# Kernel optimization log

Measured on AMD Instinct MI355X. Metric: run time of the kernel, lower is better.

Reference implementation:

```python
import jax, jax.numpy as jnp
import numpy as np

N_G, E_G = 76800, 307200   # gg: line graph over bonds
N_L, E_L = 38400, 153600   # lg: atom graph; E_L == 2*N_G
B = 64                     # number of molecules (equal-sized subgraphs)
H = 8                      # attention heads
BOND, ATOM, IN_E, FE1 = 40, 92, 10, 36


def _egat_layer(nfeats, efeats, src, dst, N, W_node, b_node, W_ni, W_nj, W_fij, attn, bias, Fn, Fe):
    # edge scores: gather + add (u_add_v) + edge proj + bias, leaky_relu
    f_edge = (nfeats @ W_ni)[src] + (nfeats @ W_nj)[dst] + efeats @ W_fij + bias
    f_out = jax.nn.leaky_relu(f_edge).reshape(-1, H, Fe)         # [E,H,Fe]
    e = jnp.einsum('ehf,hf->eh', f_out, attn)                     # [E,H]
    # edge softmax over incoming edges of each destination node
    m = jax.lax.stop_gradient(jax.ops.segment_max(e, dst, num_segments=N))
    ex = jnp.exp(e - m[dst])
    a = ex / jax.ops.segment_sum(ex, dst, num_segments=N)[dst]    # [E,H]
    h = (nfeats @ W_node + b_node).reshape(-1, H, Fn)             # [N,H,Fn]
    h_out = jax.ops.segment_sum(h[src] * a[:, :, None], dst, num_segments=N)
    return h_out, f_out


def setup_inputs() -> dict:
    key = jax.random.key(0)
    ks = iter(jax.random.split(key, 64))
    def lin(i, o):
        return jax.random.normal(next(ks), (i, o), jnp.float32) * (1.0 / np.sqrt(i))
    inp = {}
    inp['gg_src'] = jax.random.randint(next(ks), (E_G,), 0, N_G, jnp.int32)
    inp['gg_dst'] = jnp.concatenate([jnp.arange(N_G, dtype=jnp.int32),
                                     jax.random.randint(next(ks), (E_G - N_G,), 0, N_G, jnp.int32)])
    inp['gg_nfeat'] = jax.random.normal(next(ks), (N_G, BOND), jnp.float32)
    inp['gg_efeat'] = jax.random.normal(next(ks), (E_G, IN_E), jnp.float32)
    inp['lg_src'] = jax.random.randint(next(ks), (E_L,), 0, N_L, jnp.int32)
    inp['lg_dst'] = jnp.concatenate([jnp.arange(N_L, dtype=jnp.int32),
                                     jax.random.randint(next(ks), (E_L - N_L,), 0, N_L, jnp.int32)])
    inp['lg_nfeat'] = jax.random.normal(next(ks), (N_L, ATOM), jnp.float32)
    inp['lg_efeat'] = jax.random.normal(next(ks), (E_L, BOND), jnp.float32)
    # layer1 (on gg): in_node=BOND, in_edge=IN_E, out_node=BOND, out_edge=FE1
    inp['W_node1'] = lin(BOND, H * BOND); inp['b_node1'] = jnp.zeros((H * BOND,), jnp.float32)
    inp['W_ni1'] = lin(BOND, H * FE1); inp['W_nj1'] = lin(BOND, H * FE1)
    inp['W_fij1'] = lin(IN_E, H * FE1)
    inp['attn1'] = jax.random.normal(next(ks), (H, FE1), jnp.float32) * 0.1
    inp['bias1'] = jnp.zeros((H * FE1,), jnp.float32)
    # layers 2a/2b (on lg): in_node=ATOM, in_edge=BOND, out_node=ATOM, out_edge=BOND
    for sfx in ('2a', '2b'):
        inp['W_node' + sfx] = lin(ATOM, H * ATOM); inp['b_node' + sfx] = jnp.zeros((H * ATOM,), jnp.float32)
        inp['W_ni' + sfx] = lin(ATOM, H * BOND); inp['W_nj' + sfx] = lin(ATOM, H * BOND)
        inp['W_fij' + sfx] = lin(BOND, H * BOND)
        inp['attn' + sfx] = jax.random.normal(next(ks), (H, BOND), jnp.float32) * 0.1
        inp['bias' + sfx] = jnp.zeros((H * BOND,), jnp.float32)
    # Readout: Linear(128,128) + Sigmoid + Linear(128,1) + Sigmoid
    inp['Wr1'] = lin(ATOM + FE1, 128); inp['br1'] = jnp.zeros((128,), jnp.float32)
    inp['Wr2'] = lin(128, 1); inp['br2'] = jnp.zeros((1,), jnp.float32)
    return inp


def reference(gg_src, gg_dst, gg_nfeat, gg_efeat, lg_src, lg_dst, lg_nfeat, lg_efeat,
              W_node1, b_node1, W_ni1, W_nj1, W_fij1, attn1, bias1,
              W_node2a, b_node2a, W_ni2a, W_nj2a, W_fij2a, attn2a, bias2a,
              W_node2b, b_node2b, W_ni2b, W_nj2b, W_fij2b, attn2b, bias2b,
              Wr1, br1, Wr2, br2):
    # stage 1: EGAT on gg, then sum over heads
    n1, e1 = _egat_layer(gg_nfeat, gg_efeat, gg_src, gg_dst, N_G,
                         W_node1, b_node1, W_ni1, W_nj1, W_fij1, attn1, bias1, BOND, FE1)
    y2n = n1.sum(axis=1)       # [N_G, BOND]
    y22 = e1.sum(axis=1)       # [E_G, FE1]
    # each gg-node feature repeated twice, added to lg edge features
    ef = jnp.repeat(y2n, 2, axis=0) + lg_efeat   # [E_L, BOND]
    nf = lg_nfeat
    nf, e2 = _egat_layer(nf, ef, lg_src, lg_dst, N_L,
                         W_node2a, b_node2a, W_ni2a, W_nj2a, W_fij2a, attn2a, bias2a, ATOM, BOND)
    nf = nf.sum(axis=1); ef = e2.sum(axis=1)
    nf, e2 = _egat_layer(nf, ef, lg_src, lg_dst, N_L,
                         W_node2b, b_node2b, W_ni2b, W_nj2b, W_fij2b, attn2b, bias2b, ATOM, BOND)
    nf = nf.sum(axis=1)
    # per-subgraph average pooling (equal-size subgraphs -> reshape mean).
    # NOTE: original pool_subgraphs(y_22, gg) slices an edge-indexed tensor by node
    # counts (upstream quirk); reproduced exactly by taking the first N_G rows.
    y1 = nf.reshape(B, N_L // B, ATOM).mean(axis=1)          # [B, ATOM]
    y2 = y22[:N_G].reshape(B, N_G // B, FE1).mean(axis=1)    # [B, FE1]
    y = jnp.concatenate([y1, y2], axis=1)                     # [B, 128]
    h = jax.nn.sigmoid(y @ Wr1 + br1)
    return jax.nn.sigmoid(h @ Wr2 + br2)                      # [B, 1]
```

## Files before the change

### kernel.cpp

```cpp
#include <hip/hip_runtime.h>
#include <math.h>

#define NG 76800
#define EG 307200
#define NL 38400
#define EL 153600
#define NB 64
#define NH 8

typedef __attribute__((ext_vector_type(8))) short bf16x8;
typedef __attribute__((ext_vector_type(4))) float f32x4;
typedef unsigned short u16;

__device__ __forceinline__ float sigmoidf(float x) { return 1.f / (1.f + expf(-x)); }
__device__ __forceinline__ u16 f2bf(float x) {
    unsigned u = __float_as_uint(x);
    return (u16)((u + 0x7FFFu + ((u >> 16) & 1u)) >> 16);
}
__device__ __forceinline__ float bf2f(u16 v) { return __uint_as_float(((unsigned)v) << 16); }

__global__ __launch_bounds__(256) void convert_pad_kernel(const float* __restrict__ src,
                                                          u16* __restrict__ dst,
                                                          int M, int K, int Kpad) {
    int i = blockIdx.x * 256 + threadIdx.x;
    if (i >= M * Kpad) return;
    int m = i / Kpad, k = i - m * Kpad;
    dst[i] = (k < K) ? f2bf(src[(size_t)m * K + k]) : (u16)0;
}

__global__ __launch_bounds__(256) void wtrans_kernel(const float* __restrict__ W, int ldw,
                                                     u16* __restrict__ dst,
                                                     int K, int N, int Nalloc, int Kpad) {
    int i = blockIdx.x * 256 + threadIdx.x;
    if (i >= Nalloc * Kpad) return;
    int n = i / Kpad, k = i - n * Kpad;
    dst[i] = (n < N && k < K) ? f2bf(W[(size_t)k * ldw + n]) : (u16)0;
}

__global__ __launch_bounds__(256) void wtrans_hp_kernel(const float* __restrict__ W, int ldw,
                                                        u16* __restrict__ dst,
                                                        int K, int Kpad) {
    int i = blockIdx.x * 256 + threadIdx.x;
    if (i >= 320 * Kpad) return;
    int n = i / Kpad, k = i - n * Kpad;
    int hh = n / 40, f = n - hh * 40;
    float v = (k < K && f < 36) ? W[(size_t)k * ldw + hh * 36 + f] : 0.f;
    dst[i] = f2bf(v);
}

__global__ __launch_bounds__(256) void wtrans_cat_kernel(const float* __restrict__ W, int ldw,
                                                         u16* __restrict__ dst,
                                                         int Fin, int Fout, int Nalloc, int KIN) {
    int i = blockIdx.x * 256 + threadIdx.x;
    if (i >= Nalloc * KIN) return;
    int n = i / KIN, k = i - n * KIN;
    int h = k / Fin, f = k - h * Fin;
    float v = (n < Fout) ? W[(size_t)f * ldw + h * Fout + n] : 0.f;
    dst[i] = f2bf(v);
}

__global__ __launch_bounds__(256) void bias_headsum_kernel(const float* __restrict__ b,
                                                           float* __restrict__ outp,
                                                           int Fout, int H, int Npad) {
    int i = blockIdx.x * 256 + threadIdx.x;
    if (i >= Npad) return;
    float s = 0.f;
    if (i < Fout)
        for (int h = 0; h < H; ++h) s += b[h * Fout + i];
    outp[i] = s;
}

__global__ __launch_bounds__(256) void meta_kernel(const float* __restrict__ attn1,
                                                   const float* __restrict__ bias1,
                                                   const float* __restrict__ b2a,
                                                   const float* __restrict__ b2b,
                                                   float* __restrict__ attn_p1,
                                                   float* __restrict__ bias_cat1,
                                                   float* __restrict__ bias_cat2a,
                                                   float* __restrict__ bias_cat2b) {
    int i = blockIdx.x * 256 + threadIdx.x;
    if (i < 320) {
        int hh = i / 40, f = i - hh * 40;
        attn_p1[i] = (f < 36) ? attn1[hh * 36 + f] : 0.f;
    } else if (i < 960) {
        int j = i - 320;
        float v = 0.f;
        if (j < 320) {
            int hh = j / 40, f = j - hh * 40;
            v = (f < 36) ? bias1[hh * 36 + f] : 0.f;
        }
        bias_cat1[j] = v;
    } else if (i < 1600) {
        int j = i - 960;
        bias_cat2a[j] = (j < 320) ? b2a[j] : 0.f;
    } else if (i < 2240) {
        int j = i - 1600;
        bias_cat2b[j] = (j < 320) ? b2b[j] : 0.f;
    }
}

template <int KPAD>
__global__ __launch_bounds__(256) void gemm_bf_kernel(const u16* __restrict__ A,
                                                      const u16* __restrict__ Wt,
                                                      const float* __restrict__ bias,
                                                      u16* __restrict__ C, int Ncols,
                                                      int Nstride) {
    __shared__ u16 st[4][16 * 72];
    const int m0 = blockIdx.x * 64;
    const int n0 = blockIdx.y * 64;
    const int wv = threadIdx.x >> 6;
    const int lane = threadIdx.x & 63;
    const int q = lane >> 4;
    const int mr = lane & 15;

    const u16* Arow = A + (size_t)(m0 + wv * 16 + mr) * KPAD;
    f32x4 acc[4];
#pragma unroll
    for (int t = 0; t < 4; ++t) acc[t] = (f32x4){0.f, 0.f, 0.f, 0.f};

#pragma unroll
    for (int k0 = 0; k0 < KPAD; k0 += 32) {
        bf16x8 af = *(const bf16x8*)(Arow + k0 + q * 8);
#pragma unroll
        for (int t = 0; t < 4; ++t) {
            bf16x8 bv = *(const bf16x8*)(Wt + (size_t)(n0 + t * 16 + mr) * KPAD + k0 + q * 8);
            acc[t] = __builtin_amdgcn_mfma_f32_16x16x32_bf16(af, bv, acc[t], 0, 0, 0);
        }
    }

    u16* myst = st[wv];
#pragma unroll
    for (int t = 0; t < 4; ++t) {
        const int colme = n0 + t * 16 + mr;
        const float bb = (bias && colme < Ncols) ? bias[colme] : 0.f;
#pragma unroll
        for (int r = 0; r < 4; ++r)
            myst[(q * 4 + r) * 72 + t * 16 + mr] = f2bf(acc[t][r] + bb);
    }
    const int rrow = lane >> 3;
    const int rcol = (lane & 7) * 8;
    bf16x8 v0 = *(const bf16x8*)(myst + rrow * 72 + rcol);
    bf16x8 v1 = *(const bf16x8*)(myst + (rrow + 8) * 72 + rcol);
    const int gcol = n0 + rcol;
    if (gcol < Ncols) {
        const int grow = m0 + wv * 16 + rrow;
        *(bf16x8*)(C + (size_t)grow * Nstride + gcol) = v0;
        *(bf16x8*)(C + (size_t)(grow + 8) * Nstride + gcol) = v1;
    }
}

__global__ __launch_bounds__(256) void ef2a_kernel(const float* __restrict__ lg_ef,
                                                   const u16* __restrict__ y2n,
                                                   u16* __restrict__ dst) {
    int i = blockIdx.x * 256 + threadIdx.x;
    if (i >= EL * 64) return;
    int e = i >> 6, c = i & 63;
    dst[i] = (c < 40) ? f2bf(lg_ef[(size_t)e * 40 + c] + bf2f(y2n[(size_t)(e >> 1) * 40 + c]))
                      : (u16)0;
}

template <int KPAD, int FSMODE>
__global__ __launch_bounds__(128) void pe_edge_kernel(
    const u16* __restrict__ A,
    const u16* __restrict__ Wt,
    const int* __restrict__ src, const int* __restrict__ dst,
    const u16* __restrict__ Pn,
    const float* __restrict__ attn,
    float* __restrict__ esc,
    void* __restrict__ fsum,
    int e0, int CH, int fsumE) {
    __shared__ u16 pe[16][328];
    const int wv = threadIdx.x >> 6;
    const int lane = threadIdx.x & 63;
    const int q = lane >> 4;
    const int mr = lane & 15;
    const int m0 = blockIdx.x * 16;

    {
        const int t0 = wv * 10;
        const u16* Arow = A + (size_t)(m0 + mr) * KPAD;
        f32x4 acc[10];
#pragma unroll
        for (int t = 0; t < 10; ++t) acc[t] = (f32x4){0.f, 0.f, 0.f, 0.f};
#pragma unroll
        for (int k0 = 0; k0 < KPAD; k0 += 32) {
            bf16x8 af = *(const bf16x8*)(Arow + k0 + q * 8);
#pragma unroll
            for (int t = 0; t < 10; ++t) {
                bf16x8 bv = *(const bf16x8*)(Wt + (size_t)((t0 + t) * 16 + mr) * KPAD + k0 + q * 8);
                acc[t] = __builtin_amdgcn_mfma_f32_16x16x32_bf16(af, bv, acc[t], 0, 0, 0);
            }
        }
#pragma unroll
        for (int t = 0; t < 10; ++t)
#pragma unroll
            for (int r = 0; r < 4; ++r)
                pe[q * 4 + r][(t0 + t) * 16 + mr] = f2bf(acc[t][r]);
    }
    __syncthreads();

    const int lc = (lane < 40) ? lane : 39;
    const int h = lc / 5, o = lc - h * 5;
    const int c = h * 40 + o * 8;
    const bool act = (lane < 40);

    float attn_r[8];
#pragma unroll
    for (int j = 0; j < 8; ++j) attn_r[j] = attn[c + j];

    const int row0 = wv * 8;
    int e = e0 + m0 + row0;
    int s = src[e], d = dst[e];
    bf16x8 api = *(const bf16x8*)(Pn + (size_t)s * 640 + c);
    bf16x8 apj = *(const bf16x8*)(Pn + (size_t)d * 640 + 320 + c);

#pragma unroll
    for (int ei = 0; ei < 8; ++ei) {
        bf16x8 napi, napj;
        if (ei < 7) {
            const int ne = e + 1;
            const int ns = src[ne], nd = dst[ne];
            napi = *(const bf16x8*)(Pn + (size_t)ns * 640 + c);
            napj = *(const bf16x8*)(Pn + (size_t)nd * 640 + 320 + c);
        }
        const int row = row0 + ei;
        bf16x8 ape = *(const bf16x8*)(&pe[row][c]);

        float v[8];
        float ehp = 0.f;
#pragma unroll
        for (int j = 0; j < 8; ++j) {
            float x = bf2f((u16)api[j]) + bf2f((u16)apj[j]) + bf2f((u16)ape[j]);
            x = x > 0.f ? x : 0.01f * x;
            v[j] = x;
            ehp += x * attn_r[j];
        }
        float eh = 0.f;
#pragma unroll
        for (int k = 0; k < 5; ++k) eh += __shfl(ehp, h * 5 + k, 64);
        if (act && o == 0) esc[(size_t)e * 8 + h] = eh;

        if (FSMODE != 0 && e < fsumE) {
#pragma unroll
            for (int m = 4; m >= 1; m >>= 1) {
                const int p = (h ^ m) * 5 + o;
#pragma unroll
                for (int j = 0; j < 8; ++j) v[j] += __shfl(v[j], p, 64);
            }
            if (act && h == 0) {
#pragma unroll
                for (int j = 0; j < 8; ++j) {
                    const int f = o * 8 + j;
                    if (FSMODE == 1) {
                        if (f < 36) ((float*)fsum)[(size_t)e * 36 + f] = v[j];
                    } else {
                        ((u16*)fsum)[(size_t)e * 64 + f] = f2bf(v[j]);
                    }
                }
            }
        }
        if (ei < 7) {
            api = napi;
            apj = napj;
        }
        ++e;
    }
}

__global__ __launch_bounds__(256) void hist_kernel(const int* __restrict__ dst,
                                                   int* __restrict__ cnt, int E) {
    int i = blockIdx.x * 256 + threadIdx.x;
    if (i < E) atomicAdd(&cnt[dst[i]], 1);
}

__global__ __launch_bounds__(1024) void scan_block_kernel(const int* __restrict__ cnt,
                                                          int* __restrict__ excl,
                                                          int* __restrict__ bsum, int N) {
    __shared__ int sd[1024];
    const int tid = threadIdx.x;
    const int i = blockIdx.x * 1024 + tid;
    int v = (i < N) ? cnt[i] : 0;
    sd[tid] = v;
    __syncthreads();
    for (int off = 1; off < 1024; off <<= 1) {
        int t = (tid >= off) ? sd[tid - off] : 0;
        __syncthreads();
        sd[tid] += t;
        __syncthreads();
    }
    if (i < N) excl[i] = sd[tid] - v;
    if (tid == 1023) bsum[blockIdx.x] = sd[1023];
}

__global__ void scan_top_kernel(int* __restrict__ bsum, int nblk) {
    if (threadIdx.x == 0 && blockIdx.x == 0) {
        int run = 0;
        for (int b = 0; b < nblk; ++b) {
            int t = bsum[b];
            bsum[b] = run;
            run += t;
        }
    }
}

__global__ __launch_bounds__(256) void scan_add_kernel(int* __restrict__ row_ptr,
                                                       const int* __restrict__ bsum,
                                                       int N, int E) {
    int i = blockIdx.x * 256 + threadIdx.x;
    if (i < N) row_ptr[i] += bsum[i >> 10];
    if (i == 0) row_ptr[N] = E;
}

__global__ __launch_bounds__(256) void scatter_kernel(const int* __restrict__ dst,
                                                      const int* __restrict__ src,
                                                      const int* __restrict__ row_ptr,
                                                      int* __restrict__ cur,
                                                      int* __restrict__ eidx,
                                                      int* __restrict__ srcs, int E) {
    int i = blockIdx.x * 256 + threadIdx.x;
    if (i < E) {
        int d = dst[i];
        int pos = row_ptr[d] + atomicAdd(&cur[d], 1);
        eidx[pos] = i;
        srcs[pos] = src[i];
    }
}

template <int GH>
__global__ __launch_bounds__(256) void csr_softmax_kernel(
    const int* __restrict__ row_ptr, const int* __restrict__ eidx,
    const float* __restrict__ esc, float* __restrict__ wcsr, int N) {
    constexpr int NS = 64 / GH;
    const int wid = threadIdx.x >> 6;
    const int lane = threadIdx.x & 63;
    const int nid = blockIdx.x * 4 + wid;
    if (nid >= N) return;
    const int r0 = row_ptr[nid], r1 = row_ptr[nid + 1];
    const int h = lane & (GH - 1);
    const int slot = lane / GH;

    float mx = -1e30f;
    for (int i = r0 + slot; i < r1; i += NS)
        mx = fmaxf(mx, esc[(size_t)eidx[i] * GH + h]);
#pragma unroll
    for (int m = GH; m < 64; m <<= 1) mx = fmaxf(mx, __shfl_xor(mx, m, 64));

    float den = 0.f;
    for (int i = r0 + slot; i < r1; i += NS)
        den += expf(esc[(size_t)eidx[i] * GH + h] - mx);
#pragma unroll
    for (int m = GH; m < 64; m <<= 1) den += __shfl_xor(den, m, 64);
    const float rden = 1.f / den;

    for (int i = r0 + slot; i < r1; i += NS)
        wcsr[(size_t)i * GH + h] = expf(esc[(size_t)eidx[i] * GH + h] - mx) * rden;
}

template <int Fn, int GH, int NFS>
__global__ __launch_bounds__(256) void node_agg_raw_kernel(
    const int* __restrict__ row_ptr,
    const int* __restrict__ srcs,
    const float* __restrict__ wcsr,
    const u16* __restrict__ nf,
    u16* __restrict__ agg, int N) {
    constexpr int PAIRS = Fn / 2;
    const int wid = threadIdx.x >> 6;
    const int lane = threadIdx.x & 63;
    const int nid = blockIdx.x * 4 + wid;
    if (nid >= N) return;
    const int r0 = row_ptr[nid], r1 = row_ptr[nid + 1];
    const int col = 2 * lane;
    const bool act = (lane < PAIRS);

    float a0[GH], a1[GH];
#pragma unroll
    for (int h = 0; h < GH; ++h) { a0[h] = 0.f; a1[h] = 0.f; }

    for (int i = r0; i < r1; i += 4) {
        const u16* prs[4];
        float wv[4][GH];
#pragma unroll
        for (int b = 0; b < 4; ++b) {
            const int ii = (i + b < r1) ? (i + b) : (r1 - 1);
            prs[b] = nf + (size_t)srcs[ii] * NFS;
            const float live = (i + b < r1) ? 1.f : 0.f;
            const float* wp = wcsr + (size_t)ii * GH;
#pragma unroll
            for (int h = 0; h < GH; ++h) wv[b][h] = wp[h] * live;
        }
        if (act) {
            unsigned pv[4];
#pragma unroll
            for (int b = 0; b < 4; ++b) pv[b] = *(const unsigned*)(prs[b] + col);
#pragma unroll
            for (int b = 0; b < 4; ++b) {
                const float lo = bf2f((u16)(pv[b] & 0xFFFFu));
                const float hi = bf2f((u16)(pv[b] >> 16));
#pragma unroll
                for (int h = 0; h < GH; ++h) {
                    a0[h] += wv[b][h] * lo;
                    a1[h] += wv[b][h] * hi;
                }
            }
        }
    }
    if (act) {
        u16* ob = agg + (size_t)nid * (GH * Fn);
#pragma unroll
        for (int h = 0; h < GH; ++h) {
            unsigned pk = (unsigned)f2bf(a0[h]) | ((unsigned)f2bf(a1[h]) << 16);
            *(unsigned*)(ob + h * Fn + col) = pk;
        }
    }
}

__global__ __launch_bounds__(256) void readout_kernel(const u16* __restrict__ nfb,
                                                      const float* __restrict__ y22p,
                                                      const float* __restrict__ Wr1,
                                                      const float* __restrict__ br1,
                                                      const float* __restrict__ Wr2,
                                                      const float* __restrict__ br2,
                                                      float* __restrict__ out) {
    const int b = blockIdx.x;
    const int t = threadIdx.x;
    __shared__ float sA[20][96];
    __shared__ float sB[28][36];
    __shared__ float y[128];
    __shared__ float hh[128];
    __shared__ float red[128];
    if (t < 240) {
        const int cc = t % 12, rg = t / 12;
        float s[8];
#pragma unroll
        for (int j = 0; j < 8; ++j) s[j] = 0.f;
        const u16* base = nfb + (size_t)b * 600 * 96 + cc * 8;
        for (int i = rg; i < 600; i += 20) {
            bf16x8 v = *(const bf16x8*)(base + (size_t)i * 96);
#pragma unroll
            for (int j = 0; j < 8; ++j) s[j] += bf2f((u16)v[j]);
        }
#pragma unroll
        for (int j = 0; j < 8; ++j) sA[rg][cc * 8 + j] = s[j];
    }
    if (t < 252) {
        const int cc = t % 9, rg = t / 9;
        float s0 = 0.f, s1 = 0.f, s2 = 0.f, s3 = 0.f;
        const float* base = y22p + (size_t)b * 1200 * 36 + cc * 4;
        for (int i = rg; i < 1200; i += 28) {
            const float* p = base + (size_t)i * 36;
            s0 += p[0]; s1 += p[1]; s2 += p[2]; s3 += p[3];
        }
        sB[rg][cc * 4 + 0] = s0;
        sB[rg][cc * 4 + 1] = s1;
        sB[rg][cc * 4 + 2] = s2;
        sB[rg][cc * 4 + 3] = s3;
    }
    __syncthreads();
    if (t < 92) {
        float s = 0.f;
        for (int r = 0; r < 20; ++r) s += sA[r][t];
        y[t] = s * (1.f / 600.f);
    } else if (t >= 128 && t < 164) {
        const int f = t - 128;
        float s = 0.f;
        for (int r = 0; r < 28; ++r) s += sB[r][f];
        y[92 + f] = s * (1.f / 1200.f);
    }
    __syncthreads();
    if (t < 128) {
        float s = br1[t];
        for (int c = 0; c < 128; ++c) s += y[c] * Wr1[(size_t)c * 128 + t];
        hh[t] = sigmoidf(s);
    }
    __syncthreads();
    if (t < 128) red[t] = hh[t] * Wr2[t];
    __syncthreads();
    for (int k = 64; k > 0; k >>= 1) {
        if (t < k) red[t] += red[t + k];
        __syncthreads();
    }
    if (t == 0) out[b] = sigmoidf(red[0] + br2[0]);
}

static inline int cdiv(int a, int b) { return (a + b - 1) / b; }

extern "C" void kernel_launch(void* const* d_in, const int* in_sizes, int n_in,
                              void* d_out, int out_size, void* d_ws, size_t ws_size,
                              hipStream_t stream) {
    const int* gg_src = (const int*)d_in[0];
    const int* gg_dst = (const int*)d_in[1];
    const float* gg_nf = (const float*)d_in[2];
    const float* gg_ef = (const float*)d_in[3];
    const int* lg_src = (const int*)d_in[4];
    const int* lg_dst = (const int*)d_in[5];
    const float* lg_nf = (const float*)d_in[6];
    const float* lg_ef = (const float*)d_in[7];
    const float* W_node1 = (const float*)d_in[8];
    const float* b_node1 = (const float*)d_in[9];
    const float* W_ni1 = (const float*)d_in[10];
    const float* W_nj1 = (const float*)d_in[11];
    const float* W_fij1 = (const float*)d_in[12];
    const float* attn1 = (const float*)d_in[13];
    const float* bias1 = (const float*)d_in[14];
    const float* W_node2a = (const float*)d_in[15];
    const float* b_node2a = (const float*)d_in[16];
    const float* W_ni2a = (const float*)d_in[17];
    const float* W_nj2a = (const float*)d_in[18];
    const float* W_fij2a = (const float*)d_in[19];
    const float* attn2a = (const float*)d_in[20];
    const float* bias2a = (const float*)d_in[21];
    const float* W_node2b = (const float*)d_in[22];
    const float* b_node2b = (const float*)d_in[23];
    const float* W_ni2b = (const float*)d_in[24];
    const float* W_nj2b = (const float*)d_in[25];
    const float* W_fij2b = (const float*)d_in[26];
    const float* attn2b = (const float*)d_in[27];
    const float* bias2b = (const float*)d_in[28];
    const float* Wr1 = (const float*)d_in[29];
    const float* br1 = (const float*)d_in[30];
    const float* Wr2 = (const float*)d_in[31];
    const float* br2 = (const float*)d_in[32];
    float* out = (float*)d_out;

    char* ws = (char*)d_ws;
    size_t off = 0;
    auto take = [&](size_t bytes) {
        size_t o = off;
        off += (bytes + 255) & ~(size_t)255;
        return (void*)(ws + o);
    };
    u16* y2n = (u16*)take((size_t)NG * 40 * 2);
    float* y22p = (float*)take((size_t)NG * 36 * 4);
    float* esc = (float*)take((size_t)EG * 8 * 4);
    float* wcsr = (float*)take((size_t)EG * 8 * 4);
    int* gg_row = (int*)take((size_t)(NG + 1) * 4);
    int* gg_eidx = (int*)take((size_t)EG * 4);
    int* gg_srcs = (int*)take((size_t)EG * 4);
    int* gg_cnt = (int*)take((size_t)NG * 4);
    int* lg_row = (int*)take((size_t)(NL + 1) * 4);
    int* lg_eidx = (int*)take((size_t)EL * 4);
    int* lg_srcs = (int*)take((size_t)EL * 4);
    int* lg_cnt = (int*)take((size_t)NL * 4);
    int* bsum = (int*)take((size_t)128 * 4);
    u16* gg_nf_bf = (u16*)take((size_t)NG * 64 * 2);
    u16* gg_ef_bf = (u16*)take((size_t)EG * 32 * 2);
    u16* lg_nf_bf = (u16*)take((size_t)NL * 96 * 2);
    u16* nfa_bf = (u16*)take((size_t)NL * 96 * 2);
    u16* nfb_bf = (u16*)take((size_t)NL * 96 * 2);
    u16* ef_shared = (u16*)take((size_t)EL * 64 * 2);
    u16* wt_ninj1 = (u16*)take((size_t)640 * 64 * 2);
    u16* wt_fij1 = (u16*)take((size_t)320 * 32 * 2);
    u16* wt_ninj2a = (u16*)take((size_t)640 * 96 * 2);
    u16* wt_ninj2b = (u16*)take((size_t)640 * 96 * 2);
    u16* wt_fij2a = (u16*)take((size_t)320 * 64 * 2);
    u16* wt_fij2b = (u16*)take((size_t)320 * 64 * 2);
    u16* wt_cat1 = (u16*)take((size_t)64 * 320 * 2);
    u16* wt_cat2a = (u16*)take((size_t)128 * 736 * 2);
    u16* wt_cat2b = (u16*)take((size_t)128 * 736 * 2);
    float* bsum1 = (float*)take((size_t)64 * 4);
    float* bsum2a = (float*)take((size_t)128 * 4);
    float* bsum2b = (float*)take((size_t)128 * 4);
    float* attn_p1 = (float*)take((size_t)320 * 4);
    float* bias_cat1 = (float*)take((size_t)640 * 4);
    float* bias_cat2a = (float*)take((size_t)640 * 4);
    float* bias_cat2b = (float*)take((size_t)640 * 4);
    u16* slab = (u16*)take((size_t)NG * 640 * 2);

    auto cvt = [&](const float* s, u16* d, int M, int K, int Kpad) {
        convert_pad_kernel<<<cdiv(M * Kpad, 256), 256, 0, stream>>>(s, d, M, K, Kpad);
    };
    auto wtr = [&](const float* W, int ldw, u16* d, int K, int N, int Nalloc, int Kpad) {
        wtrans_kernel<<<cdiv(Nalloc * Kpad, 256), 256, 0, stream>>>(W, ldw, d, K, N, Nalloc, Kpad);
    };
    auto build_csr = [&](const int* dst, const int* src, int* row_ptr, int* eidx, int* srcs,
                         int* cnt, int N, int E) {
        hipMemsetAsync(cnt, 0, (size_t)N * 4, stream);
        hist_kernel<<<cdiv(E, 256), 256, 0, stream>>>(dst, cnt, E);
        int nblk = cdiv(N, 1024);
        scan_block_kernel<<<nblk, 1024, 0, stream>>>(cnt, row_ptr, bsum, N);
        scan_top_kernel<<<1, 64, 0, stream>>>(bsum, nblk);
        scan_add_kernel<<<cdiv(N, 256), 256, 0, stream>>>(row_ptr, bsum, N, E);
        hipMemsetAsync(cnt, 0, (size_t)N * 4, stream);
        scatter_kernel<<<cdiv(E, 256), 256, 0, stream>>>(dst, src, row_ptr, cnt, eidx, srcs, E);
    };

    build_csr(gg_dst, gg_src, gg_row, gg_eidx, gg_srcs, gg_cnt, NG, EG);
    build_csr(lg_dst, lg_src, lg_row, lg_eidx, lg_srcs, lg_cnt, NL, EL);

    cvt(gg_nf, gg_nf_bf, NG, 40, 64);
    cvt(gg_ef, gg_ef_bf, EG, 10, 32);
    cvt(lg_nf, lg_nf_bf, NL, 92, 96);
    wtrans_hp_kernel<<<cdiv(320 * 64, 256), 256, 0, stream>>>(W_ni1, 288, wt_ninj1, 40, 64);
    wtrans_hp_kernel<<<cdiv(320 * 64, 256), 256, 0, stream>>>(W_nj1, 288, wt_ninj1 + 320 * 64, 40, 64);
    wtrans_hp_kernel<<<cdiv(320 * 32, 256), 256, 0, stream>>>(W_fij1, 288, wt_fij1, 10, 32);
    wtr(W_ni2a, 320, wt_ninj2a, 92, 320, 320, 96);
    wtr(W_nj2a, 320, wt_ninj2a + 320 * 96, 92, 320, 320, 96);
    wtr(W_ni2b, 320, wt_ninj2b, 92, 320, 320, 96);
    wtr(W_nj2b, 320, wt_ninj2b + 320 * 96, 92, 320, 320, 96);
    wtr(W_fij2a, 320, wt_fij2a, 40, 320, 320, 64);
    wtr(W_fij2b, 320, wt_fij2b, 40, 320, 320, 64);
    wtrans_cat_kernel<<<cdiv(64 * 320, 256), 256, 0, stream>>>(W_node1, 320, wt_cat1, 40, 40, 64, 320);
    wtrans_cat_kernel<<<cdiv(128 * 736, 256), 256, 0, stream>>>(W_node2a, 736, wt_cat2a, 92, 92, 128, 736);
    wtrans_cat_kernel<<<cdiv(128 * 736, 256), 256, 0, stream>>>(W_node2b, 736, wt_cat2b, 92, 92, 128, 736);
    bias_headsum_kernel<<<1, 256, 0, stream>>>(b_node1, bsum1, 40, 8, 64);
    bias_headsum_kernel<<<1, 256, 0, stream>>>(b_node2a, bsum2a, 92, 8, 128);
    bias_headsum_kernel<<<1, 256, 0, stream>>>(b_node2b, bsum2b, 92, 8, 128);
    meta_kernel<<<cdiv(2240, 256), 256, 0, stream>>>(attn1, bias1, bias2a, bias2b,
                                                     attn_p1, bias_cat1, bias_cat2a, bias_cat2b);

    {
        u16* Pn1 = slab;
        gemm_bf_kernel<64><<<dim3(NG / 64, 10), 256, 0, stream>>>(
            gg_nf_bf, wt_ninj1, bias_cat1, Pn1, 640, 640);
        pe_edge_kernel<32, 1><<<EG / 16, 128, 0, stream>>>(
            gg_ef_bf, wt_fij1, gg_src, gg_dst, Pn1, attn_p1, esc, y22p, 0, EG, NG);
        csr_softmax_kernel<8><<<NG / 4, 256, 0, stream>>>(gg_row, gg_eidx, esc, wcsr, NG);
        u16* agg1 = slab;
        node_agg_raw_kernel<40, 8, 64><<<NG / 4, 256, 0, stream>>>(gg_row, gg_srcs, wcsr,
                                                                   gg_nf_bf, agg1, NG);
        gemm_bf_kernel<320><<<dim3(NG / 64, 1), 256, 0, stream>>>(
            agg1, wt_cat1, bsum1, y2n, 40, 40);
    }

    ef2a_kernel<<<cdiv(EL * 64, 256), 256, 0, stream>>>(lg_ef, y2n, ef_shared);

    for (int layer = 0; layer < 2; ++layer) {
        const bool a = (layer == 0);
        const u16* nf_in = a ? lg_nf_bf : nfa_bf;
        const u16* Wninj = a ? wt_ninj2a : wt_ninj2b;
        const u16* Wfij = a ? wt_fij2a : wt_fij2b;
        const u16* Wcat = a ? wt_cat2a : wt_cat2b;
        const float* bs = a ? bsum2a : bsum2b;
        const float* bcat = a ? bias_cat2a : bias_cat2b;
        const float* at = a ? attn2a : attn2b;
        u16* nf_out = a ? nfa_bf : nfb_bf;

        u16* Pn2 = slab;
        gemm_bf_kernel<96><<<dim3(NL / 64, 10), 256, 0, stream>>>(nf_in, Wninj, bcat, Pn2, 640, 640);
        if (a)
            pe_edge_kernel<64, 2><<<EL / 16, 128, 0, stream>>>(
                ef_shared, Wfij, lg_src, lg_dst, Pn2, at, esc, ef_shared, 0, EL, EL);
        else
            pe_edge_kernel<64, 0><<<EL / 16, 128, 0, stream>>>(
                ef_shared, Wfij, lg_src, lg_dst, Pn2, at, esc, nullptr, 0, EL, 0);
        csr_softmax_kernel<8><<<NL / 4, 256, 0, stream>>>(lg_row, lg_eidx, esc, wcsr, NL);
        u16* agg2 = slab;
        node_agg_raw_kernel<92, 8, 96><<<NL / 4, 256, 0, stream>>>(lg_row, lg_srcs, wcsr,
                                                                   nf_in, agg2, NL);
        gemm_bf_kernel<736><<<dim3(NL / 64, 2), 256, 0, stream>>>(
            agg2, Wcat, bs, nf_out, 96, 96);
    }

    readout_kernel<<<NB, 256, 0, stream>>>(nfb_bf, y22p, Wr1, br1, Wr2, br2, out);
}
```

Baseline: 965.5 us.

## Fuse neighbor aggregation with head-sum projection GEMM via shared-memory tile

Merges the per-node weighted aggregation kernel and the following projection GEMM into one kernel. Each block aggregates 16 nodes into an LDS tile, then runs MFMA bf16 against the concatenated head weights and writes the biased output directly. This removes the round trip of the large [N, H*Fn] aggregate buffer through global memory and one launch per layer. In exchange, each wave handles 4 nodes serially, and the MFMA phase is lightly loaded, which could reduce occupancy and latency hiding.

```diff
diff --git a/kernel.cpp b/kernel.cpp
--- a/kernel.cpp
+++ b/kernel.cpp
@@ -356,61 +356,111 @@
         wcsr[(size_t)i * GH + h] = expf(esc[(size_t)eidx[i] * GH + h] - mx) * rden;
 }
 
-template <int Fn, int GH, int NFS>
-__global__ __launch_bounds__(256) void node_agg_raw_kernel(
+template <int Fn, int GH, int NFS, int KIN, int NOUT, int NTILES>
+__global__ __launch_bounds__(256) void node_agg_gemm_kernel(
     const int* __restrict__ row_ptr,
     const int* __restrict__ srcs,
     const float* __restrict__ wcsr,
     const u16* __restrict__ nf,
-    u16* __restrict__ agg, int N) {
+    const u16* __restrict__ Wcat,
+    const float* __restrict__ bsum,
+    u16* __restrict__ outp,
+    int N) {
     constexpr int PAIRS = Fn / 2;
-    const int wid = threadIdx.x >> 6;
+    constexpr int KINP = KIN + 8;
+    __shared__ u16 tile[16][KINP];
+    __shared__ u16 ot[16][NTILES * 16];
+    const int wv = threadIdx.x >> 6;
     const int lane = threadIdx.x & 63;
-    const int nid = blockIdx.x * 4 + wid;
-    if (nid >= N) return;
-    const int r0 = row_ptr[nid], r1 = row_ptr[nid + 1];
-    const int col = 2 * lane;
-    const bool act = (lane < PAIRS);
-
-    float a0[GH], a1[GH];
-#pragma unroll
-    for (int h = 0; h < GH; ++h) { a0[h] = 0.f; a1[h] = 0.f; }
-
-    for (int i = r0; i < r1; i += 4) {
-        const u16* prs[4];
-        float wv[4][GH];
-#pragma unroll
-        for (int b = 0; b < 4; ++b) {
-            const int ii = (i + b < r1) ? (i + b) : (r1 - 1);
-            prs[b] = nf + (size_t)srcs[ii] * NFS;
-            const float live = (i + b < r1) ? 1.f : 0.f;
-            const float* wp = wcsr + (size_t)ii * GH;
-#pragma unroll
-            for (int h = 0; h < GH; ++h) wv[b][h] = wp[h] * live;
-        }
-        if (act) {
-            unsigned pv[4];
-#pragma unroll
-            for (int b = 0; b < 4; ++b) pv[b] = *(const unsigned*)(prs[b] + col);
-#pragma unroll
-            for (int b = 0; b < 4; ++b) {
-                const float lo = bf2f((u16)(pv[b] & 0xFFFFu));
-                const float hi = bf2f((u16)(pv[b] >> 16));
-#pragma unroll
-                for (int h = 0; h < GH; ++h) {
-                    a0[h] += wv[b][h] * lo;
-                    a1[h] += wv[b][h] * hi;
+    const int q = lane >> 4;
+    const int mr = lane & 15;
+    const int nblk = blockIdx.x * 16;
+
+    {
+        const int col = 2 * lane;
+        const bool act = (lane < PAIRS);
+#pragma unroll
+        for (int nn = 0; nn < 4; ++nn) {
+            const int nid = nblk + wv * 4 + nn;
+            const int r0 = row_ptr[nid], r1 = row_ptr[nid + 1];
+            float a0[GH], a1[GH];
+#pragma unroll
+            for (int h = 0; h < GH; ++h) { a0[h] = 0.f; a1[h] = 0.f; }
+            for (int i = r0; i < r1; i += 4) {
+                const u16* prs[4];
+                float wvv[4][GH];
+#pragma unroll
+                for (int b = 0; b < 4; ++b) {
+                    const int ii = (i + b < r1) ? (i + b) : (r1 - 1);
+                    prs[b] = nf + (size_t)srcs[ii] * NFS;
+                    const float live = (i + b < r1) ? 1.f : 0.f;
+                    const float* wp = wcsr + (size_t)ii * GH;
+#pragma unroll
+                    for (int h = 0; h < GH; ++h) wvv[b][h] = wp[h] * live;
+                }
+                if (act) {
+                    unsigned pv[4];
+#pragma unroll
+                    for (int b = 0; b < 4; ++b) pv[b] = *(const unsigned*)(prs[b] + col);
+#pragma unroll
+                    for (int b = 0; b < 4; ++b) {
+                        const float lo = bf2f((u16)(pv[b] & 0xFFFFu));
+                        const float hi = bf2f((u16)(pv[b] >> 16));
+#pragma unroll
+                        for (int h = 0; h < GH; ++h) {
+                            a0[h] += wvv[b][h] * lo;
+                            a1[h] += wvv[b][h] * hi;
+                        }
+                    }
                 }
             }
-        }
-    }
-    if (act) {
-        u16* ob = agg + (size_t)nid * (GH * Fn);
-#pragma unroll
-        for (int h = 0; h < GH; ++h) {
-            unsigned pk = (unsigned)f2bf(a0[h]) | ((unsigned)f2bf(a1[h]) << 16);
-            *(unsigned*)(ob + h * Fn + col) = pk;
-        }
+            if (act) {
+                u16* ob = tile[wv * 4 + nn];
+#pragma unroll
+                for (int h = 0; h < GH; ++h) {
+                    unsigned pk = (unsigned)f2bf(a0[h]) | ((unsigned)f2bf(a1[h]) << 16);
+                    *(unsigned*)(ob + h * Fn + col) = pk;
+                }
+            }
+        }
+    }
+    __syncthreads();
+
+    {
+        const int t0 = wv;
+        const int t1 = wv + 4;
+        f32x4 acc0 = (f32x4){0.f, 0.f, 0.f, 0.f};
+        f32x4 acc1 = (f32x4){0.f, 0.f, 0.f, 0.f};
+#pragma unroll
+        for (int k0 = 0; k0 < KIN; k0 += 32) {
+            bf16x8 af = *(const bf16x8*)(&tile[mr][k0 + q * 8]);
+            if (t0 < NTILES) {
+                bf16x8 bv = *(const bf16x8*)(Wcat + (size_t)(t0 * 16 + mr) * KIN + k0 + q * 8);
+                acc0 = __builtin_amdgcn_mfma_f32_16x16x32_bf16(af, bv, acc0, 0, 0, 0);
+            }
+            if (t1 < NTILES) {
+                bf16x8 bv = *(const bf16x8*)(Wcat + (size_t)(t1 * 16 + mr) * KIN + k0 + q * 8);
+                acc1 = __builtin_amdgcn_mfma_f32_16x16x32_bf16(af, bv, acc1, 0, 0, 0);
+            }
+        }
+        if (t0 < NTILES) {
+            const float bb = bsum[t0 * 16 + mr];
+#pragma unroll
+            for (int r = 0; r < 4; ++r) ot[q * 4 + r][t0 * 16 + mr] = f2bf(acc0[r] + bb);
+        }
+        if (t1 < NTILES) {
+            const float bb = bsum[t1 * 16 + mr];
+#pragma unroll
+            for (int r = 0; r < 4; ++r) ot[q * 4 + r][t1 * 16 + mr] = f2bf(acc1[r] + bb);
+        }
+    }
+    __syncthreads();
+
+    constexpr int DW = NOUT / 2;
+    for (int idx = threadIdx.x; idx < 16 * DW; idx += 256) {
+        const int row = idx / DW, c2 = idx - row * DW;
+        unsigned pk = *(const unsigned*)(&ot[row][c2 * 2]);
+        *(unsigned*)(outp + (size_t)(nblk + row) * NOUT + c2 * 2) = pk;
     }
 }
 
@@ -615,11 +665,8 @@
         pe_edge_kernel<32, 1><<<EG / 16, 128, 0, stream>>>(
             gg_ef_bf, wt_fij1, gg_src, gg_dst, Pn1, attn_p1, esc, y22p, 0, EG, NG);
         csr_softmax_kernel<8><<<NG / 4, 256, 0, stream>>>(gg_row, gg_eidx, esc, wcsr, NG);
-        u16* agg1 = slab;
-        node_agg_raw_kernel<40, 8, 64><<<NG / 4, 256, 0, stream>>>(gg_row, gg_srcs, wcsr,
-                                                                   gg_nf_bf, agg1, NG);
-        gemm_bf_kernel<320><<<dim3(NG / 64, 1), 256, 0, stream>>>(
-            agg1, wt_cat1, bsum1, y2n, 40, 40);
+        node_agg_gemm_kernel<40, 8, 64, 320, 40, 3><<<NG / 16, 256, 0, stream>>>(
+            gg_row, gg_srcs, wcsr, gg_nf_bf, wt_cat1, bsum1, y2n, NG);
     }
 
     ef2a_kernel<<<cdiv(EL * 64, 256), 256, 0, stream>>>(lg_ef, y2n, ef_shared);
@@ -644,11 +691,8 @@
             pe_edge_kernel<64, 0><<<EL / 16, 128, 0, stream>>>(
                 ef_shared, Wfij, lg_src, lg_dst, Pn2, at, esc, nullptr, 0, EL, 0);
         csr_softmax_kernel<8><<<NL / 4, 256, 0, stream>>>(lg_row, lg_eidx, esc, wcsr, NL);
-        u16* agg2 = slab;
-        node_agg_raw_kernel<92, 8, 96><<<NL / 4, 256, 0, stream>>>(lg_row, lg_srcs, wcsr,
-                                                                   nf_in, agg2, NL);
-        gemm_bf_kernel<736><<<dim3(NL / 64, 2), 256, 0, stream>>>(
-            agg2, Wcat, bs, nf_out, 96, 96);
+        node_agg_gemm_kernel<92, 8, 96, 736, 96, 6><<<NL / 16, 256, 0, stream>>>(
+            lg_row, lg_srcs, wcsr, nf_in, Wcat, bs, nf_out, NL);
     }
 
     readout_kernel<<<NB, 256, 0, stream>>>(nfb_bf, y22p, Wr1, br1, Wr2, br2, out);
```

Result: faster. 908.1 us (-6.0%).
